# Kernel optimization log

Measured on AMD Instinct MI355X. Metric: run time of the kernel, lower is better.

The kernel has to match this reference:

```python
import jax, jax.numpy as jnp
import numpy as np

D, H, DFF, MD = 1024, 16, 4096, 128
B, TS, TT = 8, 512, 512
EPS = 1e-6


def _ln(x, s, b):
    m = jnp.mean(x, axis=-1, keepdims=True)
    v = jnp.mean((x - m) ** 2, axis=-1, keepdims=True)
    return (x - m) * jax.lax.rsqrt(v + EPS) * s + b


def _rel_bias(emb, qlen, klen):
    # T5-style bidirectional bucket: [H, qlen, klen]
    q = jnp.arange(qlen)[:, None]
    k = jnp.arange(klen)[None, :]
    rp = k - q
    bucket = jnp.where(rp < 0, jnp.minimum(-rp, MD - 1), jnp.minimum(rp, MD - 1) + MD)
    return emb[bucket].transpose(2, 0, 1)


def _mha(xq, xkv, w_in, b_in, w_out, b_out, bias):
    # nn.MultiheadAttention math: packed in_proj [3D,D], additive attn bias [H,Tq,Tk]
    Bq, Tq, _ = xq.shape
    Tk = xkv.shape[1]
    hd = D // H
    wq, wk, wv = jnp.split(w_in, 3, axis=0)
    bq, bk, bv = jnp.split(b_in, 3, axis=0)
    q = (xq @ wq.T + bq).reshape(Bq, Tq, H, hd).transpose(0, 2, 1, 3)
    k = (xkv @ wk.T + bk).reshape(Bq, Tk, H, hd).transpose(0, 2, 1, 3)
    v = (xkv @ wv.T + bv).reshape(Bq, Tk, H, hd).transpose(0, 2, 1, 3)
    scores = jnp.einsum('bhqd,bhkd->bhqk', q, k) / jnp.sqrt(jnp.asarray(hd, xq.dtype))
    scores = scores + bias[None]
    attn = jax.nn.softmax(scores, axis=-1)
    out = jnp.einsum('bhqk,bhkd->bhqd', attn, v)
    out = out.transpose(0, 2, 1, 3).reshape(Bq, Tq, D)
    return out @ w_out.T + b_out


def setup_inputs() -> dict:
    key = jax.random.key(0)
    ks = jax.random.split(key, 40)
    std = 0.02

    def n(i, shape):
        return jax.random.normal(ks[i], shape, dtype=jnp.float32) * std

    return {
        'src': jax.random.normal(ks[0], (B, TS, D), dtype=jnp.float32),
        'tgt': jax.random.normal(ks[1], (B, TT, D), dtype=jnp.float32),
        # encoder layer
        'enc_in_w': n(2, (3 * D, D)), 'enc_in_b': jnp.zeros((3 * D,)),
        'enc_out_w': n(3, (D, D)), 'enc_out_b': jnp.zeros((D,)),
        'enc_ff1_w': n(4, (DFF, D)), 'enc_ff1_b': jnp.zeros((DFF,)),
        'enc_ff2_w': n(5, (D, DFF)), 'enc_ff2_b': jnp.zeros((D,)),
        'enc_n1_s': jnp.ones((D,)), 'enc_n1_b': jnp.zeros((D,)),
        'enc_n2_s': jnp.ones((D,)), 'enc_n2_b': jnp.zeros((D,)),
        'enc_rel': n(6, (2 * MD, H)),
        # decoder layer
        'dec_sa_in_w': n(7, (3 * D, D)), 'dec_sa_in_b': jnp.zeros((3 * D,)),
        'dec_sa_out_w': n(8, (D, D)), 'dec_sa_out_b': jnp.zeros((D,)),
        'dec_ca_in_w': n(9, (3 * D, D)), 'dec_ca_in_b': jnp.zeros((3 * D,)),
        'dec_ca_out_w': n(10, (D, D)), 'dec_ca_out_b': jnp.zeros((D,)),
        'dec_ff1_w': n(11, (DFF, D)), 'dec_ff1_b': jnp.zeros((DFF,)),
        'dec_ff2_w': n(12, (D, DFF)), 'dec_ff2_b': jnp.zeros((D,)),
        'dec_n1_s': jnp.ones((D,)), 'dec_n1_b': jnp.zeros((D,)),
        'dec_n2_s': jnp.ones((D,)), 'dec_n2_b': jnp.zeros((D,)),
        'dec_n3_s': jnp.ones((D,)), 'dec_n3_b': jnp.zeros((D,)),
        'dec_rel_self': n(13, (2 * MD, H)),
        'dec_rel_cross': n(14, (2 * MD, H)),
    }


def reference(src, tgt,
              enc_in_w, enc_in_b, enc_out_w, enc_out_b,
              enc_ff1_w, enc_ff1_b, enc_ff2_w, enc_ff2_b,
              enc_n1_s, enc_n1_b, enc_n2_s, enc_n2_b, enc_rel,
              dec_sa_in_w, dec_sa_in_b, dec_sa_out_w, dec_sa_out_b,
              dec_ca_in_w, dec_ca_in_b, dec_ca_out_w, dec_ca_out_b,
              dec_ff1_w, dec_ff1_b, dec_ff2_w, dec_ff2_b,
              dec_n1_s, dec_n1_b, dec_n2_s, dec_n2_b, dec_n3_s, dec_n3_b,
              dec_rel_self, dec_rel_cross):
    Ts, Tt = src.shape[1], tgt.shape[1]

    # ---- encoder layer (pre-LN) ----
    eb = _rel_bias(enc_rel, Ts, Ts)  # [H,Ts,Ts]
    x = src
    x = x + _mha(_ln(x, enc_n1_s, enc_n1_b), _ln(x, enc_n1_s, enc_n1_b),
                 enc_in_w, enc_in_b, enc_out_w, enc_out_b, eb)
    h = _ln(x, enc_n2_s, enc_n2_b)
    x = x + (jax.nn.relu(h @ enc_ff1_w.T + enc_ff1_b) @ enc_ff2_w.T + enc_ff2_b)
    memory = x

    # ---- decoder layer (pre-LN) ----
    causal = jnp.where(jnp.arange(Tt)[None, :] > jnp.arange(Tt)[:, None], -jnp.inf, 0.0)
    sb = _rel_bias(dec_rel_self, Tt, Tt) + causal[None]  # [H,Tt,Tt]
    cb = _rel_bias(dec_rel_cross, Tt, Ts)                # [H,Tt,Ts]
    y = tgt
    yn = _ln(y, dec_n1_s, dec_n1_b)
    y = y + _mha(yn, yn, dec_sa_in_w, dec_sa_in_b, dec_sa_out_w, dec_sa_out_b, sb)
    y = y + _mha(_ln(y, dec_n2_s, dec_n2_b), memory,
                 dec_ca_in_w, dec_ca_in_b, dec_ca_out_w, dec_ca_out_b, cb)
    h = _ln(y, dec_n3_s, dec_n3_b)
    y = y + (jax.nn.relu(h @ dec_ff1_w.T + dec_ff1_b) @ dec_ff2_w.T + dec_ff2_b)
    return y
```

## Files before the change

kernel.cpp:

```cpp
#include <hip/hip_runtime.h>

using u16 = unsigned short;

typedef float f32x4 __attribute__((ext_vector_type(4)));
typedef __bf16 bf16x8v __attribute__((ext_vector_type(8)));
typedef bf16x8v bf16x8 __attribute__((may_alias));
typedef u16 u16x8v __attribute__((ext_vector_type(8)));
typedef u16x8v u16x8 __attribute__((may_alias));
typedef u16 u16x4v __attribute__((ext_vector_type(4)));
typedef u16x4v u16x4 __attribute__((may_alias));
typedef float f32x4v __attribute__((ext_vector_type(4)));
typedef f32x4v float4a __attribute__((may_alias));

#define GPTR(p) ((__attribute__((address_space(1))) void*)(p))
#define LPTR(p) ((__attribute__((address_space(3))) void*)(p))

__device__ __forceinline__ u16 f2bf(float f) {
  unsigned u = __builtin_bit_cast(unsigned, f);
  u += 0x7FFFu + ((u >> 16) & 1u);
  return (u16)(u >> 16);
}

__device__ __forceinline__ f32x4 mfma16(bf16x8 a, bf16x8 b, f32x4 c) {
  return __builtin_amdgcn_mfma_f32_16x16x32_bf16(a, b, c, 0, 0, 0);
}

struct Srcs { const float* s[10]; };

__global__ __launch_bounds__(256) void cvt_all(Srcs srcs, u16* __restrict__ dst) {
  constexpr int off[11] = {0, 786432, 1048576, 2097152, 3145728,
                           3932160, 4194304, 4980736, 5242880, 6291456, 7340032};
  const int i = blockIdx.x * 256 + threadIdx.x;
  int r = 0;
#pragma unroll
  for (int j = 1; j < 10; j++) r += (i >= off[j]);
  float4a v = ((const float4a*)srcs.s[r])[i - off[r]];
  u16x4 o;
  o[0] = f2bf(v[0]); o[1] = f2bf(v[1]); o[2] = f2bf(v[2]); o[3] = f2bf(v[3]);
  ((u16x4*)dst)[i] = o;
}

__global__ __launch_bounds__(256) void add_cvt(const float* __restrict__ a,
                                               const float* __restrict__ b,
                                               u16* __restrict__ o) {
  const int i = blockIdx.x * 256 + threadIdx.x;
  float4a va = ((const float4a*)a)[i];
  float4a vb = ((const float4a*)b)[i];
  u16x4 ov;
#pragma unroll
  for (int j = 0; j < 4; j++) ov[j] = f2bf(va[j] + vb[j]);
  ((u16x4*)o)[i] = ov;
}

__global__ __launch_bounds__(256) void add_f32(float* __restrict__ o,
                                               const float* __restrict__ b) {
  const int i = blockIdx.x * 256 + threadIdx.x;
  float4a vo = ((float4a*)o)[i];
  float4a vb = ((const float4a*)b)[i];
#pragma unroll
  for (int j = 0; j < 4; j++) vo[j] += vb[j];
  ((float4a*)o)[i] = vo;
}

__global__ __launch_bounds__(256) void ln_k(const float* __restrict__ x,
                                            const float* __restrict__ sc,
                                            const float* __restrict__ bi,
                                            u16* __restrict__ out) {
  const int row = blockIdx.x, tid = threadIdx.x;
  float4a v = ((const float4a*)(x + (size_t)row * 1024))[tid];
  float s1 = v[0] + v[1] + v[2] + v[3];
  float s2 = v[0]*v[0] + v[1]*v[1] + v[2]*v[2] + v[3]*v[3];
#pragma unroll
  for (int off = 32; off; off >>= 1) { s1 += __shfl_xor(s1, off); s2 += __shfl_xor(s2, off); }
  __shared__ float red[8];
  if ((tid & 63) == 0) { red[tid >> 6] = s1; red[4 + (tid >> 6)] = s2; }
  __syncthreads();
  s1 = red[0] + red[1] + red[2] + red[3];
  s2 = red[4] + red[5] + red[6] + red[7];
  const float mean = s1 * (1.f / 1024.f);
  const float rstd = rsqrtf(s2 * (1.f / 1024.f) - mean * mean + 1e-6f);
  float4a s4 = ((const float4a*)sc)[tid];
  float4a b4 = ((const float4a*)bi)[tid];
  u16x4 o;
#pragma unroll
  for (int j = 0; j < 4; j++) o[j] = f2bf((v[j] - mean) * rstd * s4[j] + b4[j]);
  ((u16x4*)(out + (size_t)row * 1024))[tid] = o;
}

template <int BN_T, int MW, int EPI, int PF>
__global__ __launch_bounds__(256) void gemm_bt(
    const u16* __restrict__ A, int lda,
    const u16* __restrict__ W, int ldw,
    const float* __restrict__ bias,
    const float* __restrict__ C0, int ldc0,
    void* __restrict__ outv, int ldo, int K,
    float* __restrict__ part) {
  constexpr int BM = 128, BK = 64;
  constexpr int NW = 4 / MW;
  constexpr int FM = BM / MW / 16;
  constexpr int FN = BN_T / NW / 16;
  constexpr int RA = (BM * BK * 2) / 4096;
  constexpr int RB = (BN_T * BK * 2) / 4096;
  constexpr int NB = PF ? 2 : 1;
  __shared__ alignas(16) u16 As[NB][BM * BK];
  __shared__ alignas(16) u16 Bs[NB][BN_T * BK];
  const int tid = threadIdx.x, lane = tid & 63, wv = tid >> 6;
  const int kb = (EPI == 3) ? blockIdx.z * K : 0;

  const int gx = gridDim.x;
  const int nwg = gx * gridDim.y;
  const int orig = blockIdx.y * gx + blockIdx.x;
  const int qq = nwg >> 3, rr = nwg & 7;
  const int xcd = orig & 7, idx = orig >> 3;
  const int wg = (xcd < rr ? xcd * (qq + 1) : rr * (qq + 1) + (xcd - rr) * qq) + idx;
  const int bm = (wg / gx) * BM, bn = (wg % gx) * BN_T;

  const int wr = (wv / NW) * (BM / MW);
  const int wc = (wv % NW) * (BN_T / NW);
  const int la = lane & 15, lg = lane >> 4;
  const int r7 = la & 7;
  const int srow = wv * 8 + (lane >> 3);
  const int scol = ((lane & 7) ^ (lane >> 3)) << 3;
  const u16* gA = A + (size_t)(bm + srow) * lda + scol;
  const u16* gB = W + (size_t)(bn + srow) * ldw + scol;

  f32x4 acc[FM][FN] = {};

  auto stage = [&](int buf, int k0) {
#pragma unroll
    for (int r = 0; r < RA; r++)
      __builtin_amdgcn_global_load_lds(GPTR(gA + (size_t)r * 32 * lda + k0),
                                       LPTR(&As[buf][(wv * 8 + r * 32) * BK]), 16, 0, 0);
#pragma unroll
    for (int r = 0; r < RB; r++)
      __builtin_amdgcn_global_load_lds(GPTR(gB + (size_t)r * 32 * ldw + k0),
                                       LPTR(&Bs[buf][(wv * 8 + r * 32) * BK]), 16, 0, 0);
  };

  auto compute = [&](int buf) {
#pragma unroll
    for (int kk = 0; kk < BK; kk += 32) {
      const int off = ((((kk >> 3) + lg) ^ r7) << 3);
      bf16x8 af[FM], bfr[FN];
#pragma unroll
      for (int m = 0; m < FM; m++)
        af[m] = *(const bf16x8*)&As[buf][(wr + m * 16 + la) * BK + off];
#pragma unroll
      for (int n = 0; n < FN; n++)
        bfr[n] = *(const bf16x8*)&Bs[buf][(wc + n * 16 + la) * BK + off];
#pragma unroll
      for (int m = 0; m < FM; m++)
#pragma unroll
        for (int n = 0; n < FN; n++)
          acc[m][n] = mfma16(af[m], bfr[n], acc[m][n]);
    }
  };

  if constexpr (PF) {
    stage(0, kb);
    int buf = 0;
    const int NT = K / BK;
    for (int t = 0; t < NT; ++t) {
      if (t + 1 < NT) {
        stage(buf ^ 1, kb + (t + 1) * BK);
        if constexpr (RA + RB == 8)
          asm volatile("s_waitcnt vmcnt(8)" ::: "memory");
        else
          asm volatile("s_waitcnt vmcnt(6)" ::: "memory");
      } else {
        asm volatile("s_waitcnt vmcnt(0)" ::: "memory");
      }
      __builtin_amdgcn_s_barrier();
      __builtin_amdgcn_sched_barrier(0);
      compute(buf);
      __builtin_amdgcn_s_barrier();
      buf ^= 1;
    }
  } else {
    for (int k0 = 0; k0 < K; k0 += BK) {
      __syncthreads();
      stage(0, kb + k0);
      __syncthreads();
      compute(0);
    }
  }

  const bool addb = (EPI != 3) || (blockIdx.z == 0);
  float bv[FN];
#pragma unroll
  for (int n = 0; n < FN; n++) bv[n] = addb ? bias[bn + wc + n * 16 + la] : 0.f;
#pragma unroll
  for (int m = 0; m < FM; m++) {
#pragma unroll
    for (int j = 0; j < 4; j++) {
      const int row = bm + wr + m * 16 + (lane >> 4) * 4 + j;
#pragma unroll
      for (int n = 0; n < FN; n++) {
        const int col = bn + wc + n * 16 + la;
        float v = acc[m][n][j] + bv[n];
        if constexpr (EPI == 1) v = fmaxf(v, 0.f);
        if constexpr (EPI == 2) {
          ((float*)outv)[(size_t)row * ldo + col] = v + C0[(size_t)row * ldc0 + col];
        } else if constexpr (EPI == 3) {
          if (blockIdx.z == 0)
            ((float*)outv)[(size_t)row * ldo + col] = v + C0[(size_t)row * ldc0 + col];
          else
            part[(size_t)row * ldo + col] = v;
        } else {
          ((u16*)outv)[(size_t)row * ldo + col] = f2bf(v);
        }
      }
    }
  }
}

__global__ __launch_bounds__(512) void gemm256_relu(
    const u16* __restrict__ A, int lda,
    const u16* __restrict__ W, int ldw,
    const float* __restrict__ bias,
    u16* __restrict__ out, int ldo, int K) {
  __shared__ alignas(16) u16 As[2][256 * 64];
  __shared__ alignas(16) u16 Bs[2][256 * 64];
  const int tid = threadIdx.x, lane = tid & 63, wid = tid >> 6;
  const int wm = wid >> 2, wn = wid & 3;
  const int gx = gridDim.x;
  const int nwg = gx * gridDim.y;
  const int orig = blockIdx.y * gx + blockIdx.x;
  const int qq = nwg >> 3, rr = nwg & 7;
  const int xcd = orig & 7, idx = orig >> 3;
  const int wg = (xcd < rr ? xcd * (qq + 1) : rr * (qq + 1) + (xcd - rr) * qq) + idx;
  const int bm = (wg / gx) * 256, bn = (wg % gx) * 256;

  const int la = lane & 15, lg = lane >> 4, r7 = la & 7;
  const int srow = tid >> 3;
  const int scol = ((tid & 7) ^ (srow & 7)) << 3;
  const u16* gA = A + (size_t)(bm + srow) * lda + scol;
  const u16* gB = W + (size_t)(bn + srow) * ldw + scol;

  f32x4 acc[8][4] = {};

#define STG(ARR, GP, LD, buf, k0, h)                                               \
  {                                                                                \
    _Pragma("unroll")                                                              \
    for (int r = 2 * (h); r < 2 * (h) + 2; r++)                                    \
      __builtin_amdgcn_global_load_lds(GPTR(GP + (size_t)(r * 64) * LD + (k0)),    \
                                       LPTR(&ARR[buf][(r * 64 + wid * 8) * 64]),   \
                                       16, 0, 0);                                  \
  }
#define RDB(buf, kk)                                                               \
  _Pragma("unroll")                                                                \
  for (int nf = 0; nf < 4; nf++)                                                   \
    Br[nf] = *(const bf16x8*)&Bs[buf][(wn * 64 + nf * 16 + la) * 64 +              \
                                      (((((kk) >> 3) + lg) ^ r7) << 3)];
#define RDA(buf, kk, mh)                                                           \
  _Pragma("unroll")                                                                \
  for (int mi = 0; mi < 4; mi++)                                                   \
    Ar[mi] = *(const bf16x8*)&As[buf][(wm * 128 + ((mh) * 4 + mi) * 16 + la) * 64 +\
                                      (((((kk) >> 3) + lg) ^ r7) << 3)];
#define MM(mh)                                                                     \
  __builtin_amdgcn_s_barrier();                                                    \
  asm volatile("s_waitcnt lgkmcnt(0)" ::: "memory");                               \
  __builtin_amdgcn_sched_barrier(0);                                               \
  __builtin_amdgcn_s_setprio(1);                                                   \
  _Pragma("unroll")                                                                \
  for (int mi = 0; mi < 4; mi++)                                                   \
    _Pragma("unroll")                                                              \
    for (int nf = 0; nf < 4; nf++)                                                 \
      acc[(mh) * 4 + mi][nf] = mfma16(Ar[mi], Br[nf], acc[(mh) * 4 + mi][nf]);     \
  __builtin_amdgcn_s_setprio(0);                                                   \
  __builtin_amdgcn_s_barrier();

  STG(As, gA, lda, 0, 0, 0) STG(As, gA, lda, 0, 0, 1)
  STG(Bs, gB, ldw, 0, 0, 0) STG(Bs, gB, ldw, 0, 0, 1)
  asm volatile("s_waitcnt vmcnt(0)" ::: "memory");
  __builtin_amdgcn_s_barrier();

  const int NIT = K >> 7;
  for (int it = 0; it < NIT; ++it) {
    const int k1 = it * 128 + 64;
    const int k2 = it * 128 + 128;
    const bool more = (it + 1 < NIT);
    bf16x8 Ar[4], Br[4];

    RDB(0, 0) RDA(0, 0, 0) STG(As, gA, lda, 1, k1, 0)
    __builtin_amdgcn_sched_barrier(0);
    MM(0)
    RDA(0, 0, 1) STG(As, gA, lda, 1, k1, 1)
    __builtin_amdgcn_sched_barrier(0);
    MM(1)
    RDB(0, 32) RDA(0, 32, 1) STG(Bs, gB, ldw, 1, k1, 0)
    __builtin_amdgcn_sched_barrier(0);
    MM(1)
    RDA(0, 32, 0) STG(Bs, gB, ldw, 1, k1, 1)
    __builtin_amdgcn_sched_barrier(0);
    asm volatile("s_waitcnt vmcnt(0)" ::: "memory");
    MM(0)
    RDB(1, 0) RDA(1, 0, 0) if (more) STG(As, gA, lda, 0, k2, 0)
    __builtin_amdgcn_sched_barrier(0);
    MM(0)
    RDA(1, 0, 1) if (more) STG(As, gA, lda, 0, k2, 1)
    __builtin_amdgcn_sched_barrier(0);
    MM(1)
    RDB(1, 32) RDA(1, 32, 1) if (more) STG(Bs, gB, ldw, 0, k2, 0)
    __builtin_amdgcn_sched_barrier(0);
    MM(1)
    RDA(1, 32, 0) if (more) STG(Bs, gB, ldw, 0, k2, 1)
    __builtin_amdgcn_sched_barrier(0);
    if (more) { asm volatile("s_waitcnt vmcnt(0)" ::: "memory"); }
    MM(0)
  }
#undef STG
#undef RDB
#undef RDA
#undef MM

  float bv[4];
#pragma unroll
  for (int nf = 0; nf < 4; nf++) bv[nf] = bias[bn + wn * 64 + nf * 16 + la];
#pragma unroll
  for (int mf = 0; mf < 8; mf++)
#pragma unroll
    for (int j = 0; j < 4; j++) {
      const int row = bm + wm * 128 + mf * 16 + lg * 4 + j;
#pragma unroll
      for (int nf = 0; nf < 4; nf++) {
        const int col = bn + wn * 64 + nf * 16 + la;
        float v = fmaxf(acc[mf][nf][j] + bv[nf], 0.f);
        out[(size_t)row * ldo + col] = f2bf(v);
      }
    }
}

template <bool CAUSAL>
__global__ __launch_bounds__(256) void attn_k(
    const u16* __restrict__ Qb, int ldq,
    const u16* __restrict__ Kb, int ldk,
    const u16* __restrict__ Vb, int ldv,
    const float* __restrict__ rel,
    u16* __restrict__ Ob, int ldo,
    int Tq, int Tk) {
  __shared__ alignas(16) u16 Ks[128 * 64];
  __shared__ alignas(16) u16 Vt[64 * 136];
  __shared__ alignas(16) u16 Ps[4][16 * 40];
  __shared__ float biasl[256];
  const int tid = threadIdx.x, lane = tid & 63, w = tid >> 6;
  const int b = blockIdx.y >> 4, h = blockIdx.y & 15;
  const int q0 = blockIdx.x * 64;
  const int la = lane & 15, lg = lane >> 4, r7 = la & 7;

  biasl[tid] = rel[tid * 16 + h];

  const int qr0 = q0 + w * 16;
  const u16* qp = Qb + (size_t)(b * Tq + qr0 + la) * ldq + h * 64 + lg * 8;
  const bf16x8 qf0 = *(const bf16x8*)qp;
  const bf16x8 qf1 = *(const bf16x8*)(qp + 32);

  float sm[4] = {0.f, 0.f, 0.f, 0.f};
  f32x4 acc[4] = {};

  const int kv_end = CAUSAL ? (q0 + 64) : Tk;
  const int scolK = ((lane & 7) ^ (lane >> 3)) << 3;
  const u16* gK = Kb + (size_t)(b * Tk + w * 8 + (lane >> 3)) * ldk + h * 64 + scolK;
  const int vrow = tid >> 3;
  const int vcol = (tid & 7) * 8;
  const int vsw = (tid & 3) * 8;
  const u16* gV = Vb + (size_t)(b * Tk + vrow) * ldv + h * 64 + vcol;
  u16* Pw = Ps[w];

  for (int kv0 = 0; kv0 < kv_end; kv0 += 128) {
    __syncthreads();
#pragma unroll
    for (int r = 0; r < 4; r++)
      __builtin_amdgcn_global_load_lds(GPTR(gK + (size_t)(kv0 + r * 32) * ldk),
                                       LPTR(&Ks[(w * 8 + r * 32) * 64]), 16, 0, 0);
    u16x8 vreg[4];
#pragma unroll
    for (int r = 0; r < 4; r++)
      vreg[r] = *(const u16x8*)(gV + (size_t)(kv0 + r * 32) * ldv);
    asm volatile("s_waitcnt vmcnt(0)" ::: "memory");
#pragma unroll
    for (int r = 0; r < 4; r++) {
      const int rsw = (r * 32 + vrow) ^ vsw;
#pragma unroll
      for (int j = 0; j < 8; j++) Vt[(vcol + j) * 136 + rsw] = vreg[r][j];
    }
    __syncthreads();

#pragma unroll
    for (int sIdx = 0; sIdx < 4; sIdx++) {
#pragma unroll
      for (int half = 0; half < 2; half++) {
        const int kvt = sIdx * 2 + half;
        const bf16x8 kf0 = *(const bf16x8*)&Ks[(kvt * 16 + la) * 64 + ((lg ^ r7) << 3)];
        const bf16x8 kf1 = *(const bf16x8*)&Ks[(kvt * 16 + la) * 64 + (((4 + lg) ^ r7) << 3)];
        f32x4 t2 = {};
        t2 = mfma16(qf0, kf0, t2);
        t2 = mfma16(qf1, kf1, t2);
        const int kc = kv0 + kvt * 16 + la;
#pragma unroll
        for (int j = 0; j < 4; j++) {
          const int qr = qr0 + lg * 4 + j;
          const int rp = kc - qr;
          const int bucket = rp < 0 ? (rp > -127 ? -rp : 127) : (rp < 127 ? rp : 127) + 128;
          float sv = t2[j] * 0.125f + biasl[bucket];
          if (CAUSAL && kc > qr) sv = -30.f;
          const float p = __expf(sv);
          sm[j] += p;
          Pw[(lg * 4 + j) * 40 + half * 16 + la] = f2bf(p);
        }
      }
      const bf16x8 pf = *(const bf16x8*)&Pw[la * 40 + lg * 8];
#pragma unroll
      for (int n = 0; n < 4; n++) {
        const int dd = n * 16 + la;
        const int cc = (sIdx * 32 + lg * 8) ^ (((dd >> 3) & 3) * 8);
        const bf16x8 vf = *(const bf16x8*)&Vt[dd * 136 + cc];
        acc[n] = mfma16(pf, vf, acc[n]);
      }
    }
  }
#pragma unroll
  for (int j = 0; j < 4; j++) {
#pragma unroll
    for (int off = 1; off < 16; off <<= 1) sm[j] += __shfl_xor(sm[j], off);
  }
#pragma unroll
  for (int n = 0; n < 4; n++)
#pragma unroll
    for (int j = 0; j < 4; j++) {
      const int qr = qr0 + lg * 4 + j;
      Ob[(size_t)(b * Tq + qr) * ldo + h * 64 + n * 16 + la] = f2bf(acc[n][j] / sm[j]);
    }
}

extern "C" void kernel_launch(void* const* d_in, const int* in_sizes, int n_in,
                              void* d_out, int out_size, void* d_ws, size_t ws_size,
                              hipStream_t stream) {
  (void)in_sizes; (void)n_in; (void)out_size; (void)ws_size;
  const float* src       = (const float*)d_in[0];
  const float* tgt       = (const float*)d_in[1];
  const float* enc_in_w  = (const float*)d_in[2];
  const float* enc_in_b  = (const float*)d_in[3];
  const float* enc_out_w = (const float*)d_in[4];
  const float* enc_out_b = (const float*)d_in[5];
  const float* enc_ff1_w = (const float*)d_in[6];
  const float* enc_ff1_b = (const float*)d_in[7];
  const float* enc_ff2_w = (const float*)d_in[8];
  const float* enc_ff2_b = (const float*)d_in[9];
  const float* enc_n1_s  = (const float*)d_in[10];
  const float* enc_n1_b  = (const float*)d_in[11];
  const float* enc_n2_s  = (const float*)d_in[12];
  const float* enc_n2_b  = (const float*)d_in[13];
  const float* enc_rel   = (const float*)d_in[14];
  const float* dsa_in_w  = (const float*)d_in[15];
  const float* dsa_in_b  = (const float*)d_in[16];
  const float* dsa_out_w = (const float*)d_in[17];
  const float* dsa_out_b = (const float*)d_in[18];
  const float* dca_in_w  = (const float*)d_in[19];
  const float* dca_in_b  = (const float*)d_in[20];
  const float* dca_out_w = (const float*)d_in[21];
  const float* dca_out_b = (const float*)d_in[22];
  const float* dff1_w    = (const float*)d_in[23];
  const float* dff1_b    = (const float*)d_in[24];
  const float* dff2_w    = (const float*)d_in[25];
  const float* dff2_b    = (const float*)d_in[26];
  const float* dn1_s     = (const float*)d_in[27];
  const float* dn1_b     = (const float*)d_in[28];
  const float* dn2_s     = (const float*)d_in[29];
  const float* dn2_b     = (const float*)d_in[30];
  const float* dn3_s     = (const float*)d_in[31];
  const float* dn3_b     = (const float*)d_in[32];
  const float* drel_s    = (const float*)d_in[33];
  const float* drel_c    = (const float*)d_in[34];
  float* fo = (float*)d_out;

  char* w8 = (char*)d_ws;
  float* x_ws  = (float*)(w8 + 0);
  u16* ln_buf  = (u16*)(w8 + 16777216);
  u16* qkv     = (u16*)(w8 + 25165824);
  u16* attn_o  = (u16*)(w8 + 50331648);
  u16* ffh     = qkv;
  u16* memb    = (u16*)(w8 + 58720256);
  u16* wb      = (u16*)(w8 + 67108864);

  u16* w_enc_in  = wb;
  u16* w_enc_out = wb + 3145728;
  u16* w_enc_f1  = wb + 4194304;
  u16* w_enc_f2  = wb + 8388608;
  u16* w_dsa_in  = wb + 12582912;
  u16* w_dsa_out = wb + 15728640;
  u16* w_dca_in  = wb + 16777216;
  u16* w_dca_out = wb + 19922944;
  u16* w_dff1    = wb + 20971520;
  u16* w_dff2    = wb + 25165824;

  Srcs srcs = {{enc_in_w, enc_out_w, enc_ff1_w, enc_ff2_w, dsa_in_w,
                dsa_out_w, dca_in_w, dca_out_w, dff1_w, dff2_w}};
  cvt_all<<<dim3(28672), 256, 0, stream>>>(srcs, wb);

  ln_k<<<dim3(4096), 256, 0, stream>>>(src, enc_n1_s, enc_n1_b, ln_buf);
  gemm_bt<128,2,0,0><<<dim3(24, 32), 256, 0, stream>>>(ln_buf, 1024, w_enc_in, 1024, enc_in_b, nullptr, 0, qkv, 3072, 1024, nullptr);
  attn_k<false><<<dim3(8, 128), 256, 0, stream>>>(qkv, 3072, qkv + 1024, 3072, qkv + 2048, 3072, enc_rel, attn_o, 1024, 512, 512);
  gemm_bt<64,4,2,1><<<dim3(16, 32), 256, 0, stream>>>(attn_o, 1024, w_enc_out, 1024, enc_out_b, src, 1024, x_ws, 1024, 1024, nullptr);
  ln_k<<<dim3(4096), 256, 0, stream>>>(x_ws, enc_n2_s, enc_n2_b, ln_buf);
  gemm256_relu<<<dim3(16, 16), 512, 0, stream>>>(ln_buf, 1024, w_enc_f1, 1024, enc_ff1_b, ffh, 4096, 1024);
  gemm_bt<128,2,3,1><<<dim3(8, 32, 2), 256, 0, stream>>>(ffh, 4096, w_enc_f2, 4096, enc_ff2_b, x_ws, 1024, x_ws, 1024, 2048, fo);
  add_cvt<<<dim3(4096), 256, 0, stream>>>(x_ws, fo, memb);

  ln_k<<<dim3(4096), 256, 0, stream>>>(tgt, dn1_s, dn1_b, ln_buf);
  gemm_bt<128,2,0,0><<<dim3(24, 32), 256, 0, stream>>>(ln_buf, 1024, w_dsa_in, 1024, dsa_in_b, nullptr, 0, qkv, 3072, 1024, nullptr);
  attn_k<true><<<dim3(8, 128), 256, 0, stream>>>(qkv, 3072, qkv + 1024, 3072, qkv + 2048, 3072, drel_s, attn_o, 1024, 512, 512);
  gemm_bt<64,4,2,1><<<dim3(16, 32), 256, 0, stream>>>(attn_o, 1024, w_dsa_out, 1024, dsa_out_b, tgt, 1024, fo, 1024, 1024, nullptr);

  ln_k<<<dim3(4096), 256, 0, stream>>>(fo, dn2_s, dn2_b, ln_buf);
  gemm_bt<64,4,0,1><<<dim3(16, 32), 256, 0, stream>>>(ln_buf, 1024, w_dca_in, 1024, dca_in_b, nullptr, 0, qkv, 3072, 1024, nullptr);
  gemm_bt<128,2,0,0><<<dim3(16, 32), 256, 0, stream>>>(memb, 1024, w_dca_in + 1048576, 1024, dca_in_b + 1024, nullptr, 0, qkv + 1024, 3072, 1024, nullptr);
  attn_k<false><<<dim3(8, 128), 256, 0, stream>>>(qkv, 3072, qkv + 1024, 3072, qkv + 2048, 3072, drel_c, attn_o, 1024, 512, 512);
  gemm_bt<64,4,2,1><<<dim3(16, 32), 256, 0, stream>>>(attn_o, 1024, w_dca_out, 1024, dca_out_b, fo, 1024, fo, 1024, 1024, nullptr);

  ln_k<<<dim3(4096), 256, 0, stream>>>(fo, dn3_s, dn3_b, ln_buf);
  gemm256_relu<<<dim3(16, 16), 512, 0, stream>>>(ln_buf, 1024, w_dff1, 1024, dff1_b, ffh, 4096, 1024);
  gemm_bt<128,2,3,1><<<dim3(8, 32, 2), 256, 0, stream>>>(ffh, 4096, w_dff2, 4096, dff2_b, fo, 1024, fo, 1024, 2048, x_ws);
  add_f32<<<dim3(4096), 256, 0, stream>>>(fo, x_ws);
}
```

Measured before the change: 576.9 us.

## Reschedule 256-tile GEMM prefetch and reuse it for QKV projections

The 256x256 GEMM kernel is templated on its epilogue so it can also produce plain bf16 output without ReLU. Its prefetch schedule changes: each stage's A and B tiles are now issued in two larger bursts early in the half-iteration, and the vmcnt wait moves to after the last MFMA block. The encoder QKV, decoder self-attention QKV and cross-attention KV projections now use this larger-tile kernel instead of the 128-tile gemm_bt. Larger tiles cut global traffic per FLOP, but the grids shrink to 192 or 128 workgroups, which may underfill the CUs, and the earlier loads add pressure on memory in flight.

```diff
diff --git a/kernel.cpp b/kernel.cpp
--- a/kernel.cpp
+++ b/kernel.cpp
@@ -214,7 +214,8 @@
   }
 }
 
-__global__ __launch_bounds__(512) void gemm256_relu(
+template <int EPI>
+__global__ __launch_bounds__(512) void gemm256(
     const u16* __restrict__ A, int lda,
     const u16* __restrict__ W, int ldw,
     const float* __restrict__ bias,
@@ -239,10 +240,10 @@
 
   f32x4 acc[8][4] = {};
 
-#define STG(ARR, GP, LD, buf, k0, h)                                               \
+#define STG4(ARR, GP, LD, buf, k0)                                                 \
   {                                                                                \
     _Pragma("unroll")                                                              \
-    for (int r = 2 * (h); r < 2 * (h) + 2; r++)                                    \
+    for (int r = 0; r < 4; r++)                                                    \
       __builtin_amdgcn_global_load_lds(GPTR(GP + (size_t)(r * 64) * LD + (k0)),    \
                                        LPTR(&ARR[buf][(r * 64 + wid * 8) * 64]),   \
                                        16, 0, 0);                                  \
@@ -257,7 +258,7 @@
   for (int mi = 0; mi < 4; mi++)                                                   \
     Ar[mi] = *(const bf16x8*)&As[buf][(wm * 128 + ((mh) * 4 + mi) * 16 + la) * 64 +\
                                       (((((kk) >> 3) + lg) ^ r7) << 3)];
-#define MM(mh)                                                                     \
+#define MMCORE(mh)                                                                 \
   __builtin_amdgcn_s_barrier();                                                    \
   asm volatile("s_waitcnt lgkmcnt(0)" ::: "memory");                               \
   __builtin_amdgcn_sched_barrier(0);                                               \
@@ -267,52 +268,58 @@
     _Pragma("unroll")                                                              \
     for (int nf = 0; nf < 4; nf++)                                                 \
       acc[(mh) * 4 + mi][nf] = mfma16(Ar[mi], Br[nf], acc[(mh) * 4 + mi][nf]);     \
-  __builtin_amdgcn_s_setprio(0);                                                   \
+  __builtin_amdgcn_s_setprio(0);
+#define MM(mh)                                                                     \
+  MMCORE(mh)                                                                       \
   __builtin_amdgcn_s_barrier();
-
-  STG(As, gA, lda, 0, 0, 0) STG(As, gA, lda, 0, 0, 1)
-  STG(Bs, gB, ldw, 0, 0, 0) STG(Bs, gB, ldw, 0, 0, 1)
+#define MMW(mh)  \
+  MMCORE(mh)                                                                       \
+  asm volatile("s_waitcnt vmcnt(0)" ::: "memory");                                 \
+  __builtin_amdgcn_s_barrier();
+
+  STG4(As, gA, lda, 0, 0)
+  STG4(Bs, gB, ldw, 0, 0)
   asm volatile("s_waitcnt vmcnt(0)" ::: "memory");
   __builtin_amdgcn_s_barrier();
 
   const int NIT = K >> 7;
   for (int it = 0; it < NIT; ++it) {
-    const int k1 = it * 128 + 64;
-    const int k2 = it * 128 + 128;
+    const int kO = it * 128 + 64;
+    const int kE2 = it * 128 + 128;
     const bool more = (it + 1 < NIT);
     bf16x8 Ar[4], Br[4];
 
-    RDB(0, 0) RDA(0, 0, 0) STG(As, gA, lda, 1, k1, 0)
+    RDB(0, 0) RDA(0, 0, 0) STG4(As, gA, lda, 1, kO)
     __builtin_amdgcn_sched_barrier(0);
     MM(0)
-    RDA(0, 0, 1) STG(As, gA, lda, 1, k1, 1)
+    RDA(0, 0, 1) STG4(Bs, gB, ldw, 1, kO)
     __builtin_amdgcn_sched_barrier(0);
     MM(1)
-    RDB(0, 32) RDA(0, 32, 1) STG(Bs, gB, ldw, 1, k1, 0)
+    RDB(0, 32) RDA(0, 32, 1)
     __builtin_amdgcn_sched_barrier(0);
     MM(1)
-    RDA(0, 32, 0) STG(Bs, gB, ldw, 1, k1, 1)
-    __builtin_amdgcn_sched_barrier(0);
-    asm volatile("s_waitcnt vmcnt(0)" ::: "memory");
+    RDA(0, 32, 0)
+    __builtin_amdgcn_sched_barrier(0);
+    MMW(0)
+    RDB(1, 0) RDA(1, 0, 0) if (more) STG4(As, gA, lda, 0, kE2)
+    __builtin_amdgcn_sched_barrier(0);
     MM(0)
-    RDB(1, 0) RDA(1, 0, 0) if (more) STG(As, gA, lda, 0, k2, 0)
-    __builtin_amdgcn_sched_barrier(0);
-    MM(0)
-    RDA(1, 0, 1) if (more) STG(As, gA, lda, 0, k2, 1)
+    RDA(1, 0, 1) if (more) STG4(Bs, gB, ldw, 0, kE2)
     __builtin_amdgcn_sched_barrier(0);
     MM(1)
-    RDB(1, 32) RDA(1, 32, 1) if (more) STG(Bs, gB, ldw, 0, k2, 0)
+    RDB(1, 32) RDA(1, 32, 1)
     __builtin_amdgcn_sched_barrier(0);
     MM(1)
-    RDA(1, 32, 0) if (more) STG(Bs, gB, ldw, 0, k2, 1)
-    __builtin_amdgcn_sched_barrier(0);
-    if (more) { asm volatile("s_waitcnt vmcnt(0)" ::: "memory"); }
-    MM(0)
+    RDA(1, 32, 0)
+    __builtin_amdgcn_sched_barrier(0);
+    MMW(0)
   }
-#undef STG
+#undef STG4
 #undef RDB
 #undef RDA
+#undef MMCORE
 #undef MM
+#undef MMW
 
   float bv[4];
 #pragma unroll
@@ -325,7 +332,8 @@
 #pragma unroll
       for (int nf = 0; nf < 4; nf++) {
         const int col = bn + wn * 64 + nf * 16 + la;
-        float v = fmaxf(acc[mf][nf][j] + bv[nf], 0.f);
+        float v = acc[mf][nf][j] + bv[nf];
+        if constexpr (EPI == 1) v = fmaxf(v, 0.f);
         out[(size_t)row * ldo + col] = f2bf(v);
       }
     }
@@ -499,27 +507,27 @@
   cvt_all<<<dim3(28672), 256, 0, stream>>>(srcs, wb);
 
   ln_k<<<dim3(4096), 256, 0, stream>>>(src, enc_n1_s, enc_n1_b, ln_buf);
-  gemm_bt<128,2,0,0><<<dim3(24, 32), 256, 0, stream>>>(ln_buf, 1024, w_enc_in, 1024, enc_in_b, nullptr, 0, qkv, 3072, 1024, nullptr);
+  gemm256<0><<<dim3(12, 16), 512, 0, stream>>>(ln_buf, 1024, w_enc_in, 1024, enc_in_b, qkv, 3072, 1024);
   attn_k<false><<<dim3(8, 128), 256, 0, stream>>>(qkv, 3072, qkv + 1024, 3072, qkv + 2048, 3072, enc_rel, attn_o, 1024, 512, 512);
   gemm_bt<64,4,2,1><<<dim3(16, 32), 256, 0, stream>>>(attn_o, 1024, w_enc_out, 1024, enc_out_b, src, 1024, x_ws, 1024, 1024, nullptr);
   ln_k<<<dim3(4096), 256, 0, stream>>>(x_ws, enc_n2_s, enc_n2_b, ln_buf);
-  gemm256_relu<<<dim3(16, 16), 512, 0, stream>>>(ln_buf, 1024, w_enc_f1, 1024, enc_ff1_b, ffh, 4096, 1024);
+  gemm256<1><<<dim3(16, 16), 512, 0, stream>>>(ln_buf, 1024, w_enc_f1, 1024, enc_ff1_b, ffh, 4096, 1024);
   gemm_bt<128,2,3,1><<<dim3(8, 32, 2), 256, 0, stream>>>(ffh, 4096, w_enc_f2, 4096, enc_ff2_b, x_ws, 1024, x_ws, 1024, 2048, fo);
   add_cvt<<<dim3(4096), 256, 0, stream>>>(x_ws, fo, memb);
 
   ln_k<<<dim3(4096), 256, 0, stream>>>(tgt, dn1_s, dn1_b, ln_buf);
-  gemm_bt<128,2,0,0><<<dim3(24, 32), 256, 0, stream>>>(ln_buf, 1024, w_dsa_in, 1024, dsa_in_b, nullptr, 0, qkv, 3072, 1024, nullptr);
+  gemm256<0><<<dim3(12, 16), 512, 0, stream>>>(ln_buf, 1024, w_dsa_in, 1024, dsa_in_b, qkv, 3072, 1024);
   attn_k<true><<<dim3(8, 128), 256, 0, stream>>>(qkv, 3072, qkv + 1024, 3072, qkv + 2048, 3072, drel_s, attn_o, 1024, 512, 512);
   gemm_bt<64,4,2,1><<<dim3(16, 32), 256, 0, stream>>>(attn_o, 1024, w_dsa_out, 1024, dsa_out_b, tgt, 1024, fo, 1024, 1024, nullptr);
 
   ln_k<<<dim3(4096), 256, 0, stream>>>(fo, dn2_s, dn2_b, ln_buf);
   gemm_bt<64,4,0,1><<<dim3(16, 32), 256, 0, stream>>>(ln_buf, 1024, w_dca_in, 1024, dca_in_b, nullptr, 0, qkv, 3072, 1024, nullptr);
-  gemm_bt<128,2,0,0><<<dim3(16, 32), 256, 0, stream>>>(memb, 1024, w_dca_in + 1048576, 1024, dca_in_b + 1024, nullptr, 0, qkv + 1024, 3072, 1024, nullptr);
+  gemm256<0><<<dim3(8, 16), 512, 0, stream>>>(memb, 1024, w_dca_in + 1048576, 1024, dca_in_b + 1024, qkv + 1024, 3072, 1024);
   attn_k<false><<<dim3(8, 128), 256, 0, stream>>>(qkv, 3072, qkv + 1024, 3072, qkv + 2048, 3072, drel_c, attn_o, 1024, 512, 512);
   gemm_bt<64,4,2,1><<<dim3(16, 32), 256, 0, stream>>>(attn_o, 1024, w_dca_out, 1024, dca_out_b, fo, 1024, fo, 1024, 1024, nullptr);
 
   ln_k<<<dim3(4096), 256, 0, stream>>>(fo, dn3_s, dn3_b, ln_buf);
-  gemm256_relu<<<dim3(16, 16), 512, 0, stream>>>(ln_buf, 1024, w_dff1, 1024, dff1_b, ffh, 4096, 1024);
+  gemm256<1><<<dim3(16, 16), 512, 0, stream>>>(ln_buf, 1024, w_dff1, 1024, dff1_b, ffh, 4096, 1024);
   gemm_bt<128,2,3,1><<<dim3(8, 32, 2), 256, 0, stream>>>(ffh, 4096, w_dff2, 4096, dff2_b, fo, 1024, fo, 1024, 2048, x_ws);
   add_f32<<<dim3(4096), 256, 0, stream>>>(fo, x_ws);
 }
```

Measured after the change: 563.4 us. -2.3%, faster.
